# Optimization experiments

Measured on AMD Instinct MI355X. Metric: run time of the kernel, lower is better.

The kernel has to match this reference:

```python
import jax, jax.numpy as jnp
import numpy as np

B, N, C, H = 2, 2048, 1024, 16
D = C // H
EPS = 1e-5  # torch LayerNorm default


def layernorm(x, gamma, beta):
    mu = jnp.mean(x, axis=-1, keepdims=True)
    var = jnp.mean(jnp.square(x - mu), axis=-1, keepdims=True)
    return (x - mu) * jax.lax.rsqrt(var + EPS) * gamma + beta


def setup_inputs() -> dict:
    key = jax.random.key(0)
    ks = jax.random.split(key, 4)
    x = jax.random.normal(ks[0], (B, N, C), dtype=jnp.float32)
    w_qkv = jax.random.normal(ks[1], (3 * C, C), dtype=jnp.float32) * (C ** -0.5)
    w_proj = jax.random.normal(ks[2], (C, C), dtype=jnp.float32) * (C ** -0.5)
    return {
        "x": x,
        "w_qkv": w_qkv,
        "q_gamma": jnp.ones((C,), jnp.float32),
        "q_beta": jnp.zeros((C,), jnp.float32),
        "k_gamma": jnp.ones((C,), jnp.float32),
        "k_beta": jnp.zeros((C,), jnp.float32),
        "lpe_w": jnp.ones((C,), jnp.float32),
        "lpe_b": jnp.zeros((C,), jnp.float32),
        "w_proj": w_proj,
        "b_proj": jnp.zeros((C,), jnp.float32),
    }


def reference(x, w_qkv, q_gamma, q_beta, k_gamma, k_beta, lpe_w, lpe_b, w_proj, b_proj):
    b, n, c = x.shape
    scale = D ** -0.5
    qkv = jnp.einsum('bnc,fc->bnf', x, w_qkv)            # (B,N,3C)
    qkv = qkv.reshape(b, n, 3, H, D)
    q, k, v = qkv[:, :, 0], qkv[:, :, 1], qkv[:, :, 2]   # (B,N,H,D)
    # QK-norm: LayerNorm over flattened heads (dim C)
    q = layernorm(q.reshape(b, n, c), q_gamma, q_beta).reshape(b, n, H, D)
    k = layernorm(k.reshape(b, n, c), k_gamma, k_beta).reshape(b, n, H, D)
    # LPE: depthwise 1x1x1 conv == per-channel affine on v
    v_lpe = v.reshape(b, n, c) * lpe_w + lpe_b           # (B,N,C)
    # attention
    attn = jnp.einsum('bqhd,bkhd->bhqk', q * scale, k)   # (B,H,N,N)
    attn = jax.nn.softmax(attn, axis=-1)
    out = jnp.einsum('bhqk,bkhd->bqhd', attn, v).reshape(b, n, c)
    y = jnp.einsum('bnc,oc->bno', out + v_lpe, w_proj) + b_proj
    return y
```

## Files before the change

### kernel.cpp

```cpp
#include <hip/hip_runtime.h>
#include <stdint.h>

#define Bdim 2
#define Ndim 2048
#define Cdim 1024
#define Hdim 16
#define Ddim 64
#define Fdim 3072
#define Mdim 4096

typedef unsigned int  u32;
typedef unsigned short u16;
typedef float f32x4 __attribute__((ext_vector_type(4)));
typedef short s16x8 __attribute__((ext_vector_type(8)));
typedef unsigned short u16x4 __attribute__((ext_vector_type(4)));
typedef unsigned int u32x2 __attribute__((ext_vector_type(2)));

__device__ __forceinline__ u16 f2b(float f) {
  u32 u = __builtin_bit_cast(u32, f);
  u += 0x7FFFu + ((u >> 16) & 1u);
  return (u16)(u >> 16);
}
__device__ __forceinline__ float b2f(u16 h) {
  return __builtin_bit_cast(float, (u32)h << 16);
}
__device__ __forceinline__ u32 cvtpk(float a, float b) {
  u32 d;
  asm("v_cvt_pk_bf16_f32 %0, %1, %2" : "=v"(d) : "v"(a), "v"(b));
  return d;
}
__device__ __forceinline__ f32x4 mfma16(s16x8 a, s16x8 b, f32x4 c) {
  return __builtin_amdgcn_mfma_f32_16x16x32_bf16(a, b, c, 0, 0, 0);
}
__device__ __forceinline__ void gl_lds16(const void* g, void* l) {
  __builtin_amdgcn_global_load_lds(
      (const __attribute__((address_space(1))) void*)g,
      (__attribute__((address_space(3))) void*)l, 16, 0, 0);
}
__device__ __forceinline__ bool is_bf16(const void* qg) {
  return *(const u32*)qg == 0x3F803F80u;
}

__global__ __launch_bounds__(256)
void k_prep(const void* x, const void* wq, const void* wp,
            const void* g0, const void* g1, const void* g2, const void* g3,
            const void* g4, const void* g5, const void* g6,
            u16* xb, u16* wqb, u16* wpb, float* prm) {
  const int i = blockIdx.x * 256 + threadIdx.x;
  const bool isbf = is_bf16(g0);
  const void* src; u16* dst; int k;
  if (i < 1048576)      { src = x;  dst = xb;  k = i; }
  else if (i < 1835008) { src = wq; dst = wqb; k = i - 1048576; }
  else if (i < 2097152) { src = wp; dst = wpb; k = i - 1835008; }
  else {
    const int j = i - 2097152;
    if (j >= 1792) return;
    const int fi = j * 4;
    const int pi = fi >> 10, off = fi & 1023;
    const void* s = (pi == 0) ? g0 : (pi == 1) ? g1 : (pi == 2) ? g2
                  : (pi == 3) ? g3 : (pi == 4) ? g4 : (pi == 5) ? g5 : g6;
    float4 v;
    if (isbf) {
      u16x4 h = *(const u16x4*)((const u16*)s + off);
      v.x = b2f(h.x); v.y = b2f(h.y); v.z = b2f(h.z); v.w = b2f(h.w);
    } else {
      v = *(const float4*)((const float*)s + off);
    }
    *(float4*)(prm + fi) = v;
    return;
  }
  if (isbf) {
    ((u16x4*)dst)[k] = ((const u16x4*)src)[k];
  } else {
    float4 v = ((const float4*)src)[k];
    u16x4 o;
    o.x = f2b(v.x); o.y = f2b(v.y); o.z = f2b(v.z); o.w = f2b(v.w);
    ((u16x4*)dst)[k] = o;
  }
}

template <int EPI>
__global__ __launch_bounds__(256)
void k_gemm_bt(const u16* __restrict__ A, const u16* __restrict__ W,
               u16* __restrict__ Cb, void* __restrict__ Cout,
               u16* __restrict__ vTp,
               const float* __restrict__ bias, const void* __restrict__ qg,
               int Msz, int Nsz, int Ksz) {
  __shared__ __align__(16) char lds[32768];
  const int tid = threadIdx.x;
  const int lane = tid & 63;
  const int wm = (tid >> 6) >> 1, wn = (tid >> 6) & 1;
  const int g = lane >> 4, cl = lane & 15;
  const int row0 = blockIdx.y * 128, col0 = blockIdx.x * 128;
  const int KT = Ksz >> 5;

  f32x4 acc[4][4] = {};

  auto stage = [&](int buf, int kt) {
    const int k0 = kt << 5;
#pragma unroll
    for (int iss = 0; iss < 2; ++iss) {
      const int t = iss * 256 + tid;
      const int r = t >> 2;
      const int ss = (t & 3) ^ ((r >> 1) & 3);
      gl_lds16(A + (size_t)(row0 + r) * Ksz + k0 + ss * 8, &lds[buf * 16384 + t * 16]);
      gl_lds16(W + (size_t)(col0 + r) * Ksz + k0 + ss * 8, &lds[buf * 16384 + 8192 + t * 16]);
    }
  };

  stage(0, 0);
  __syncthreads();
  int cur = 0;
  for (int kt = 0; kt < KT; ++kt) {
    if (kt + 1 < KT) stage(cur ^ 1, kt + 1);
    const char* Ab = &lds[cur * 16384];
    const char* Bb = &lds[cur * 16384 + 8192];
    s16x8 af[4], bfr[4];
#pragma unroll
    for (int mi = 0; mi < 4; ++mi) {
      const int r = wm * 64 + mi * 16 + cl;
      const int s = g ^ ((r >> 1) & 3);
      af[mi] = *(const s16x8*)(Ab + r * 64 + s * 16);
    }
#pragma unroll
    for (int nj = 0; nj < 4; ++nj) {
      const int r = wn * 64 + nj * 16 + cl;
      const int s = g ^ ((r >> 1) & 3);
      bfr[nj] = *(const s16x8*)(Bb + r * 64 + s * 16);
    }
#pragma unroll
    for (int mi = 0; mi < 4; ++mi)
#pragma unroll
      for (int nj = 0; nj < 4; ++nj)
        acc[mi][nj] = mfma16(af[mi], bfr[nj], acc[mi][nj]);
    __syncthreads();
    cur ^= 1;
  }

  const u32 oflag = (EPI == 1) ? (is_bf16(qg) ? 1u : 0u) : 0u;
#pragma unroll
  for (int mi = 0; mi < 4; ++mi)
#pragma unroll
    for (int nj = 0; nj < 4; ++nj) {
      const int m0 = row0 + wm * 64 + mi * 16 + g * 4;
      const int nbase = col0 + wn * 64 + nj * 16;
      const int n = nbase + cl;
      if (EPI == 2 && nbase >= 2048) {
        const int h = (nbase - 2048) >> 6;
        const int d = ((nbase - 2048) & 63) + cl;
        u16x4 pk;
#pragma unroll
        for (int r = 0; r < 4; ++r) pk[r] = f2b(acc[mi][nj][r]);
        *(u16x4*)(vTp + (size_t)h * (64 * 4096) + (size_t)d * 4096 + m0) = pk;
      } else {
#pragma unroll
        for (int r = 0; r < 4; ++r) {
          const int m = m0 + r;
          float v = acc[mi][nj][r];
          if (EPI == 2) {
            Cb[(size_t)m * Nsz + n] = f2b(v);
          } else {
            v += bias[n];
            if (oflag) ((u16*)Cout)[(size_t)m * Nsz + n] = f2b(v);
            else       ((float*)Cout)[(size_t)m * Nsz + n] = v;
          }
        }
      }
    }
}

__global__ __launch_bounds__(256)
void k_ln(u16* __restrict__ qkv, const float* __restrict__ prm) {
  const int m = blockIdx.x;
  const int tid = threadIdx.x;
  const int lane = tid & 63, wv = tid >> 6;
  __shared__ float red[2][4];
  u16* row = qkv + (size_t)m * Fdim;
#pragma unroll
  for (int seg = 0; seg < 2; ++seg) {
    u16* s = row + seg * 1024;
    u16x4 v = *(const u16x4*)(s + tid * 4);
    float x0 = b2f(v.x), x1 = b2f(v.y), x2 = b2f(v.z), x3 = b2f(v.w);
    float sum = x0 + x1 + x2 + x3;
    float ssq = x0 * x0 + x1 * x1 + x2 * x2 + x3 * x3;
#pragma unroll
    for (int off = 32; off >= 1; off >>= 1) {
      sum += __shfl_xor(sum, off);
      ssq += __shfl_xor(ssq, off);
    }
    if (lane == 0) { red[0][wv] = sum; red[1][wv] = ssq; }
    __syncthreads();
    const float ts = red[0][0] + red[0][1] + red[0][2] + red[0][3];
    const float tq = red[1][0] + red[1][1] + red[1][2] + red[1][3];
    __syncthreads();
    const float mu = ts * (1.0f / 1024.0f);
    const float var = tq * (1.0f / 1024.0f) - mu * mu;
    const float rstd = rsqrtf(var + 1e-5f);
    const float scl = (seg == 0) ? (0.125f * 1.4426950408889634f) : 1.0f;
    const float* gam = prm + seg * 2048;
    const float* bet = prm + seg * 2048 + 1024;
    const int c = tid * 4;
    u16x4 o;
    o.x = f2b(((x0 - mu) * rstd * gam[c + 0] + bet[c + 0]) * scl);
    o.y = f2b(((x1 - mu) * rstd * gam[c + 1] + bet[c + 1]) * scl);
    o.z = f2b(((x2 - mu) * rstd * gam[c + 2] + bet[c + 2]) * scl);
    o.w = f2b(((x3 - mu) * rstd * gam[c + 3] + bet[c + 3]) * scl);
    *(u16x4*)(s + tid * 4) = o;
  }
}

__global__ __launch_bounds__(256, 4)
void k_attn(const u16* __restrict__ qkv, const u16* __restrict__ vT,
            u16* __restrict__ pin, const float* __restrict__ prm) {
  const int bid = blockIdx.x;
  const int qt = (bid >> 3) & 31;
  const int bh = (bid & 7) * 4 + (bid >> 8);
  const int b = bh >> 4, h = bh & 15;
  const int tid = threadIdx.x, lane = tid & 63, w = tid >> 6;
  const int g = lane >> 4, cl = lane & 15;
  const int c7 = cl & 7;
  const int mrow0 = b * Ndim + qt * 64;
  const int NT = Ndim / 64;

  const u16* Qg  = qkv + (size_t)mrow0 * Fdim + h * 64;
  const u16* Kg  = qkv + (size_t)(b * Ndim) * Fdim + Cdim + h * 64;
  const u16* vTg = vT + (size_t)h * (64 * 4096) + b * Ndim;

  __shared__ __align__(16) char klds[2][8192];
  __shared__ __align__(16) char vlds[2][8192];
  __shared__ __align__(16) char plds[4][2048];

  s16x8 bq[2];
#pragma unroll
  for (int kc = 0; kc < 2; ++kc)
    bq[kc] = *(const s16x8*)(Qg + (size_t)(w * 16 + cl) * Fdim + kc * 32 + g * 8);

  f32x4 o[4] = {};
  float mr = -1e30f;
  float lr = 0.f;

  const char* akp0 = &klds[0][cl * 128 + (((0 + g) ^ c7) << 4)];
  const char* akp1 = &klds[0][cl * 128 + (((4 + g) ^ c7) << 4)];
  const char* avp0 = &vlds[0][cl * 128 + (((0 + g) ^ c7) << 4)];
  const char* avp1 = &vlds[0][cl * 128 + (((4 + g) ^ c7) << 4)];
  char* pwp[4];
#pragma unroll
  for (int nj = 0; nj < 4; ++nj)
    pwp[nj] = &plds[w][cl * 128 + ((nj * 32 + g * 8) ^ (c7 << 4))];
  const char* bpp0 = &plds[w][cl * 128 + ((0  + g * 16) ^ (c7 << 4))];
  const char* bpp1 = &plds[w][cl * 128 + ((64 + g * 16) ^ (c7 << 4))];

  const int r0 = tid >> 3;
  const int ss0 = ((tid & 7) ^ (r0 & 7)) * 8;
  const u16* kp = Kg + (size_t)r0 * Fdim + ss0;
  const u16* vp = vTg + (size_t)r0 * 4096 + ss0;
  char* kd = &klds[0][tid * 16];
  char* vd = &vlds[0][tid * 16];

  gl_lds16(kp, kd);
  gl_lds16(kp + (size_t)32 * Fdim, kd + 4096);
  gl_lds16(vp, vd);
  gl_lds16(vp + (size_t)32 * 4096, vd + 4096);
  kp += (size_t)64 * Fdim;
  vp += 64;

#define ATTN_TILE(BUF, PREFETCH)                                              \
  {                                                                           \
               \
    asm volatile("s_waitcnt vmcnt(2)" ::: "memory");                          \
    __builtin_amdgcn_s_barrier();                                             \
    __builtin_amdgcn_sched_barrier(0);                                        \
    if (PREFETCH) {                                                           \
      gl_lds16(kp, kd + ((BUF) ^ 1) * 8192);                                  \
      gl_lds16(kp + (size_t)32 * Fdim, kd + ((BUF) ^ 1) * 8192 + 4096);       \
      gl_lds16(vp, vd + ((BUF) ^ 1) * 8192);                                  \
      gl_lds16(vp + (size_t)32 * 4096, vd + ((BUF) ^ 1) * 8192 + 4096);       \
      kp += (size_t)64 * Fdim;                                                \
      vp += 64;                                                               \
    }                                                                         \
    s16x8 ak[4][2];                                                           \
    _Pragma("unroll") for (int nj = 0; nj < 4; ++nj) {                        \
      ak[nj][0] = *(const s16x8*)(akp0 + (BUF) * 8192 + nj * 2048);           \
      ak[nj][1] = *(const s16x8*)(akp1 + (BUF) * 8192 + nj * 2048);           \
    }                                                                         \
    f32x4 sv[4];                                                              \
    __builtin_amdgcn_s_setprio(1);                                            \
    _Pragma("unroll") for (int nj = 0; nj < 4; ++nj) {                        \
      f32x4 z = {0.f, 0.f, 0.f, 0.f};                                         \
      z = mfma16(ak[nj][0], bq[0], z);                                        \
      z = mfma16(ak[nj][1], bq[1], z);                                        \
      sv[nj] = z;                                                             \
    }                                                                         \
    __builtin_amdgcn_s_setprio(0);                                            \
    float a0 = fmaxf(fmaxf(sv[0][0], sv[0][1]), sv[0][2]);                    \
    float a1 = fmaxf(fmaxf(sv[0][3], sv[1][0]), sv[1][1]);                    \
    float a2 = fmaxf(fmaxf(sv[1][2], sv[1][3]), sv[2][0]);                    \
    float a3 = fmaxf(fmaxf(sv[2][1], sv[2][2]), sv[2][3]);                    \
    float a4 = fmaxf(fmaxf(sv[3][0], sv[3][1]), sv[3][2]);                    \
    float b0v = fmaxf(fmaxf(a0, a1), a2);                                     \
    float b1v = fmaxf(fmaxf(a3, a4), sv[3][3]);                               \
    float mx = fmaxf(b0v, b1v);                                               \
    if (!__all(mx <= mr + 7.0f)) {                                            \
      mx = fmaxf(mx, __shfl_xor(mx, 16));                                     \
      mx = fmaxf(mx, __shfl_xor(mx, 32));                                     \
      const float mn = fmaxf(mr, mx);                                         \
      const float corr = exp2f(mr - mn);                                      \
      mr = mn;                                                                \
      lr *= corr;                                                             \
      o[0] *= corr; o[1] *= corr; o[2] *= corr; o[3] *= corr;                 \
    }                                                                         \
    float ssum = 0.f;                                                         \
    _Pragma("unroll") for (int nj = 0; nj < 4; ++nj) {                        \
      const float p0 = exp2f(sv[nj][0] - mr), p1 = exp2f(sv[nj][1] - mr);     \
      const float p2 = exp2f(sv[nj][2] - mr), p3 = exp2f(sv[nj][3] - mr);     \
      ssum += (p0 + p1) + (p2 + p3);                                          \
      u32x2 pk2;                                                              \
      pk2.x = cvtpk(p0, p1);                                                  \
      pk2.y = cvtpk(p2, p3);                                                  \
      *(u32x2*)(pwp[nj]) = pk2;                                               \
    }                                                                         \
    lr += ssum;                                                               \
           \
    if (PREFETCH) {                                                           \
      asm volatile("s_waitcnt vmcnt(4) lgkmcnt(0)" ::: "memory");             \
    } else {                                                                  \
      asm volatile("s_waitcnt vmcnt(0) lgkmcnt(0)" ::: "memory");             \
    }                                                                         \
    __builtin_amdgcn_s_barrier();                                             \
    __builtin_amdgcn_sched_barrier(0);                                        \
    s16x8 av[4][2];                                                           \
    _Pragma("unroll") for (int dc = 0; dc < 4; ++dc) {                        \
      av[dc][0] = *(const s16x8*)(avp0 + (BUF) * 8192 + dc * 2048);           \
      av[dc][1] = *(const s16x8*)(avp1 + (BUF) * 8192 + dc * 2048);           \
    }                                                                         \
    const s16x8 bp0 = *(const s16x8*)bpp0;                                    \
    const s16x8 bp1 = *(const s16x8*)bpp1;                                    \
    __builtin_amdgcn_s_setprio(1);                                            \
    _Pragma("unroll") for (int dc = 0; dc < 4; ++dc) {                        \
      o[dc] = mfma16(av[dc][0], bp0, o[dc]);                                  \
      o[dc] = mfma16(av[dc][1], bp1, o[dc]);                                  \
    }                                                                         \
    __builtin_amdgcn_s_setprio(0);                                            \
  }

  for (int t = 0; t < NT; t += 2) {
    ATTN_TILE(0, true);
    ATTN_TILE(1, (t + 2 < NT));
  }
#undef ATTN_TILE

  {
    const int q = w * 16 + cl;
    const int m = mrow0 + q;
    const int nseq = qt * 64 + q;
    float lt = lr;
    lt += __shfl_xor(lt, 16);
    lt += __shfl_xor(lt, 32);
    const float inv = 1.0f / lt;
#pragma unroll
    for (int dc = 0; dc < 4; ++dc) {
      const int d0 = dc * 16 + g * 4;
      const int c = h * 64 + d0;
      const float4 lw = *(const float4*)(prm + 4096 + c);
      const float4 lb = *(const float4*)(prm + 5120 + c);
      float vr[4];
#pragma unroll
      for (int r = 0; r < 4; ++r) {
        const float vv = b2f(vTg[(size_t)(d0 + r) * 4096 + nseq]);
        vr[r] = o[dc][r] * inv + vv * (&lw.x)[r] + (&lb.x)[r];
      }
      u32x2 ov;
      ov.x = cvtpk(vr[0], vr[1]);
      ov.y = cvtpk(vr[2], vr[3]);
      *(u32x2*)(pin + (size_t)m * Cdim + c) = ov;
    }
  }
}

extern "C" void kernel_launch(void* const* d_in, const int* in_sizes, int n_in,
                              void* d_out, int out_size, void* d_ws, size_t ws_size,
                              hipStream_t stream) {
  (void)in_sizes; (void)n_in; (void)out_size; (void)ws_size;
  char* ws = (char*)d_ws;
  float* prm    = (float*)(ws + 256);
  u16*   xb     = (u16*)(ws + 32768);
  u16*   wqkvb  = (u16*)(ws + 32768 + 8388608);
  u16*   wprojb = (u16*)(ws + 32768 + 8388608 + 6291456);
  u16*   qkv    = (u16*)(ws + 32768 + 8388608 + 6291456 + 2097152);
  u16*   vT     = (u16*)(ws + 32768 + 8388608 + 6291456 + 2097152 + 25165824);
  u16*   pin    = xb;

  k_prep<<<8199, 256, 0, stream>>>(d_in[0], d_in[1], d_in[8],
                                   d_in[2], d_in[3], d_in[4], d_in[5],
                                   d_in[6], d_in[7], d_in[9],
                                   xb, wqkvb, wprojb, prm);

  k_gemm_bt<2><<<dim3(Fdim / 128, Mdim / 128), 256, 0, stream>>>(
      xb, wqkvb, qkv, nullptr, vT, nullptr, nullptr, Mdim, Fdim, Cdim);

  k_ln<<<Mdim, 256, 0, stream>>>(qkv, prm);

  k_attn<<<dim3(1024), 256, 0, stream>>>(qkv, vT, pin, prm);

  k_gemm_bt<1><<<dim3(Cdim / 128, Mdim / 128), 256, 0, stream>>>(
      pin, wprojb, nullptr, d_out, nullptr, prm + 6144, d_in[2], Mdim, Cdim, Cdim);
}
```

Baseline: 145.3 us.

## Double query tile per attention block to reuse K/V tiles across 128 queries

Each attention block now handles 128 query rows instead of 64, with every wave processing two 16-row query sub-blocks against the same K and V tiles loaded into LDS. This halves the number of blocks and the total K/V traffic from global memory into LDS. In exchange it roughly doubles the accumulator and score registers per thread, so the launch-bounds occupancy hint drops from 4 to 3, and with 512 blocks there may be fewer waves resident to hide latency. exp2f is also replaced by the raw hardware exp2 builtin.

```diff
diff --git a/kernel.cpp b/kernel.cpp
--- a/kernel.cpp
+++ b/kernel.cpp
@@ -29,6 +29,7 @@
   asm("v_cvt_pk_bf16_f32 %0, %1, %2" : "=v"(d) : "v"(a), "v"(b));
   return d;
 }
+__device__ __forceinline__ float rexp2(float x) { return __builtin_amdgcn_exp2f(x); }
 __device__ __forceinline__ f32x4 mfma16(s16x8 a, s16x8 b, f32x4 c) {
   return __builtin_amdgcn_mfma_f32_16x16x32_bf16(a, b, c, 0, 0, 0);
 }
@@ -209,17 +210,17 @@
   }
 }
 
-__global__ __launch_bounds__(256, 4)
+__global__ __launch_bounds__(256, 3)
 void k_attn(const u16* __restrict__ qkv, const u16* __restrict__ vT,
             u16* __restrict__ pin, const float* __restrict__ prm) {
   const int bid = blockIdx.x;
-  const int qt = (bid >> 3) & 31;
-  const int bh = (bid & 7) * 4 + (bid >> 8);
+  const int qt = (bid >> 3) & 15;
+  const int bh = (bid & 7) * 4 + (bid >> 7);
   const int b = bh >> 4, h = bh & 15;
   const int tid = threadIdx.x, lane = tid & 63, w = tid >> 6;
   const int g = lane >> 4, cl = lane & 15;
   const int c7 = cl & 7;
-  const int mrow0 = b * Ndim + qt * 64;
+  const int mrow0 = b * Ndim + qt * 128;
   const int NT = Ndim / 64;
 
   const u16* Qg  = qkv + (size_t)mrow0 * Fdim + h * 64;
@@ -228,16 +229,18 @@
 
   __shared__ __align__(16) char klds[2][8192];
   __shared__ __align__(16) char vlds[2][8192];
-  __shared__ __align__(16) char plds[4][2048];
-
-  s16x8 bq[2];
-#pragma unroll
-  for (int kc = 0; kc < 2; ++kc)
-    bq[kc] = *(const s16x8*)(Qg + (size_t)(w * 16 + cl) * Fdim + kc * 32 + g * 8);
-
-  f32x4 o[4] = {};
-  float mr = -1e30f;
-  float lr = 0.f;
+  __shared__ __align__(16) char plds[4][4096];
+
+  s16x8 bq[2][2];
+#pragma unroll
+  for (int qb = 0; qb < 2; ++qb)
+#pragma unroll
+    for (int kc = 0; kc < 2; ++kc)
+      bq[qb][kc] = *(const s16x8*)(Qg + (size_t)(w * 32 + qb * 16 + cl) * Fdim + kc * 32 + g * 8);
+
+  f32x4 o[2][4] = {};
+  float mr[2] = {-1e30f, -1e30f};
+  float lr[2] = {0.f, 0.f};
 
   const char* akp0 = &klds[0][cl * 128 + (((0 + g) ^ c7) << 4)];
   const char* akp1 = &klds[0][cl * 128 + (((4 + g) ^ c7) << 4)];
@@ -283,43 +286,47 @@
       ak[nj][0] = *(const s16x8*)(akp0 + (BUF) * 8192 + nj * 2048);           \
       ak[nj][1] = *(const s16x8*)(akp1 + (BUF) * 8192 + nj * 2048);           \
     }                                                                         \
-    f32x4 sv[4];                                                              \
-    __builtin_amdgcn_s_setprio(1);                                            \
-    _Pragma("unroll") for (int nj = 0; nj < 4; ++nj) {                        \
-      f32x4 z = {0.f, 0.f, 0.f, 0.f};                                         \
-      z = mfma16(ak[nj][0], bq[0], z);                                        \
-      z = mfma16(ak[nj][1], bq[1], z);                                        \
-      sv[nj] = z;                                                             \
-    }                                                                         \
-    __builtin_amdgcn_s_setprio(0);                                            \
-    float a0 = fmaxf(fmaxf(sv[0][0], sv[0][1]), sv[0][2]);                    \
-    float a1 = fmaxf(fmaxf(sv[0][3], sv[1][0]), sv[1][1]);                    \
-    float a2 = fmaxf(fmaxf(sv[1][2], sv[1][3]), sv[2][0]);                    \
-    float a3 = fmaxf(fmaxf(sv[2][1], sv[2][2]), sv[2][3]);                    \
-    float a4 = fmaxf(fmaxf(sv[3][0], sv[3][1]), sv[3][2]);                    \
-    float b0v = fmaxf(fmaxf(a0, a1), a2);                                     \
-    float b1v = fmaxf(fmaxf(a3, a4), sv[3][3]);                               \
-    float mx = fmaxf(b0v, b1v);                                               \
-    if (!__all(mx <= mr + 7.0f)) {                                            \
-      mx = fmaxf(mx, __shfl_xor(mx, 16));                                     \
-      mx = fmaxf(mx, __shfl_xor(mx, 32));                                     \
-      const float mn = fmaxf(mr, mx);                                         \
-      const float corr = exp2f(mr - mn);                                      \
-      mr = mn;                                                                \
-      lr *= corr;                                                             \
-      o[0] *= corr; o[1] *= corr; o[2] *= corr; o[3] *= corr;                 \
-    }                                                                         \
-    float ssum = 0.f;                                                         \
-    _Pragma("unroll") for (int nj = 0; nj < 4; ++nj) {                        \
-      const float p0 = exp2f(sv[nj][0] - mr), p1 = exp2f(sv[nj][1] - mr);     \
-      const float p2 = exp2f(sv[nj][2] - mr), p3 = exp2f(sv[nj][3] - mr);     \
-      ssum += (p0 + p1) + (p2 + p3);                                          \
-      u32x2 pk2;                                                              \
-      pk2.x = cvtpk(p0, p1);                                                  \
-      pk2.y = cvtpk(p2, p3);                                                  \
-      *(u32x2*)(pwp[nj]) = pk2;                                               \
-    }                                                                         \
-    lr += ssum;                                                               \
+    _Pragma("unroll") for (int qb = 0; qb < 2; ++qb) {                        \
+      f32x4 sv[4];                                                            \
+      __builtin_amdgcn_s_setprio(1);                                          \
+      _Pragma("unroll") for (int nj = 0; nj < 4; ++nj) {                      \
+        f32x4 z = {0.f, 0.f, 0.f, 0.f};                                       \
+        z = mfma16(ak[nj][0], bq[qb][0], z);                                  \
+        z = mfma16(ak[nj][1], bq[qb][1], z);                                  \
+        sv[nj] = z;                                                           \
+      }                                                                       \
+      __builtin_amdgcn_s_setprio(0);                                          \
+      float a0 = fmaxf(fmaxf(sv[0][0], sv[0][1]), sv[0][2]);                  \
+      float a1 = fmaxf(fmaxf(sv[0][3], sv[1][0]), sv[1][1]);                  \
+      float a2 = fmaxf(fmaxf(sv[1][2], sv[1][3]), sv[2][0]);                  \
+      float a3 = fmaxf(fmaxf(sv[2][1], sv[2][2]), sv[2][3]);                  \
+      float a4 = fmaxf(fmaxf(sv[3][0], sv[3][1]), sv[3][2]);                  \
+      float b0v = fmaxf(fmaxf(a0, a1), a2);                                   \
+      float b1v = fmaxf(fmaxf(a3, a4), sv[3][3]);                             \
+      float mx = fmaxf(b0v, b1v);                                             \
+      if (!__all(mx <= mr[qb] + 7.0f)) {                                      \
+        mx = fmaxf(mx, __shfl_xor(mx, 16));                                   \
+        mx = fmaxf(mx, __shfl_xor(mx, 32));                                   \
+        const float mn = fmaxf(mr[qb], mx);                                   \
+        const float corr = rexp2(mr[qb] - mn);                                \
+        mr[qb] = mn;                                                          \
+        lr[qb] *= corr;                                                       \
+        o[qb][0] *= corr; o[qb][1] *= corr;                                   \
+        o[qb][2] *= corr; o[qb][3] *= corr;                                   \
+      }                                                                       \
+      const float mrq = mr[qb];                                               \
+      float ssum = 0.f;                                                       \
+      _Pragma("unroll") for (int nj = 0; nj < 4; ++nj) {                      \
+        const float p0 = rexp2(sv[nj][0] - mrq), p1 = rexp2(sv[nj][1] - mrq); \
+        const float p2 = rexp2(sv[nj][2] - mrq), p3 = rexp2(sv[nj][3] - mrq); \
+        ssum += (p0 + p1) + (p2 + p3);                                        \
+        u32x2 pk2;                                                            \
+        pk2.x = cvtpk(p0, p1);                                                \
+        pk2.y = cvtpk(p2, p3);                                                \
+        *(u32x2*)(pwp[nj] + qb * 2048) = pk2;                                 \
+      }                                                                       \
+      lr[qb] += ssum;                                                         \
+    }                                                                         \
            \
     if (PREFETCH) {                                                           \
       asm volatile("s_waitcnt vmcnt(4) lgkmcnt(0)" ::: "memory");             \
@@ -333,14 +340,16 @@
       av[dc][0] = *(const s16x8*)(avp0 + (BUF) * 8192 + dc * 2048);           \
       av[dc][1] = *(const s16x8*)(avp1 + (BUF) * 8192 + dc * 2048);           \
     }                                                                         \
-    const s16x8 bp0 = *(const s16x8*)bpp0;                                    \
-    const s16x8 bp1 = *(const s16x8*)bpp1;                                    \
-    __builtin_amdgcn_s_setprio(1);                                            \
-    _Pragma("unroll") for (int dc = 0; dc < 4; ++dc) {                        \
-      o[dc] = mfma16(av[dc][0], bp0, o[dc]);                                  \
-      o[dc] = mfma16(av[dc][1], bp1, o[dc]);                                  \
-    }                                                                         \
-    __builtin_amdgcn_s_setprio(0);                                            \
+    _Pragma("unroll") for (int qb = 0; qb < 2; ++qb) {                        \
+      const s16x8 bp0 = *(const s16x8*)(bpp0 + qb * 2048);                    \
+      const s16x8 bp1 = *(const s16x8*)(bpp1 + qb * 2048);                    \
+      __builtin_amdgcn_s_setprio(1);                                          \
+      _Pragma("unroll") for (int dc = 0; dc < 4; ++dc) {                      \
+        o[qb][dc] = mfma16(av[dc][0], bp0, o[qb][dc]);                        \
+        o[qb][dc] = mfma16(av[dc][1], bp1, o[qb][dc]);                        \
+      }                                                                       \
+      __builtin_amdgcn_s_setprio(0);                                          \
+    }                                                                         \
   }
 
   for (int t = 0; t < NT; t += 2) {
@@ -349,11 +358,12 @@
   }
 #undef ATTN_TILE
 
-  {
-    const int q = w * 16 + cl;
+#pragma unroll
+  for (int qb = 0; qb < 2; ++qb) {
+    const int q = w * 32 + qb * 16 + cl;
     const int m = mrow0 + q;
-    const int nseq = qt * 64 + q;
-    float lt = lr;
+    const int nseq = qt * 128 + q;
+    float lt = lr[qb];
     lt += __shfl_xor(lt, 16);
     lt += __shfl_xor(lt, 32);
     const float inv = 1.0f / lt;
@@ -367,7 +377,7 @@
 #pragma unroll
       for (int r = 0; r < 4; ++r) {
         const float vv = b2f(vTg[(size_t)(d0 + r) * 4096 + nseq]);
-        vr[r] = o[dc][r] * inv + vv * (&lw.x)[r] + (&lb.x)[r];
+        vr[r] = o[qb][dc][r] * inv + vv * (&lw.x)[r] + (&lb.x)[r];
       }
       u32x2 ov;
       ov.x = cvtpk(vr[0], vr[1]);
@@ -400,7 +410,7 @@
 
   k_ln<<<Mdim, 256, 0, stream>>>(qkv, prm);
 
-  k_attn<<<dim3(1024), 256, 0, stream>>>(qkv, vT, pin, prm);
+  k_attn<<<dim3(512), 256, 0, stream>>>(qkv, vT, pin, prm);
 
   k_gemm_bt<1><<<dim3(Cdim / 128, Mdim / 128), 256, 0, stream>>>(
       pin, wprojb, nullptr, d_out, nullptr, prm + 6144, d_in[2], Mdim, Cdim, Cdim);
```

New measurement: 134.9 us. 1.08x faster.
